# Optimization experiments

Hardware: AMD Instinct MI355X
Metric: run time of the kernel (lower is better)

## Reference

```python
import jax, jax.numpy as jnp
import numpy as np

N = 50000        # nodes
E = 800000       # edges (before self-loops)
IN = 128         # in_dim
H = 2            # heads
C1 = 64          # hidden_dim (per head)
D1 = H * C1      # conv1 concat output = 128
OUT = 64         # out_dim
C2 = 2 * OUT     # conv2 per-head channels = 128 (concat=False -> mean over heads)
NEG = 0.2        # GATv2 leaky_relu negative slope
EPS = 1e-5       # BatchNorm eps


def setup_inputs() -> dict:
    key = jax.random.key(0)
    ks = jax.random.split(key, 14)
    s = 0.05
    inp = {
        "x": jax.random.normal(ks[0], (N, IN), jnp.float32),
        "edge_index": jax.random.randint(ks[1], (2, E), 0, N, dtype=jnp.int32),
        # conv1 (GATv2: lin_l for source, lin_r for target, att vector per head)
        "W_l1": jax.random.normal(ks[2], (IN, D1), jnp.float32) * s,
        "b_l1": jnp.zeros((D1,), jnp.float32),
        "W_r1": jax.random.normal(ks[3], (IN, D1), jnp.float32) * s,
        "b_r1": jnp.zeros((D1,), jnp.float32),
        "att1": jax.random.normal(ks[4], (H, C1), jnp.float32) * s,
        "bias1": jnp.zeros((D1,), jnp.float32),
        # batch_norm1 (affine)
        "gamma1": jnp.ones((D1,), jnp.float32),
        "beta1": jnp.zeros((D1,), jnp.float32),
        # conv2
        "W_l2": jax.random.normal(ks[5], (D1, H * C2), jnp.float32) * s,
        "b_l2": jnp.zeros((H * C2,), jnp.float32),
        "W_r2": jax.random.normal(ks[6], (D1, H * C2), jnp.float32) * s,
        "b_r2": jnp.zeros((H * C2,), jnp.float32),
        "att2": jax.random.normal(ks[7], (H, C2), jnp.float32) * s,
        "bias2": jnp.zeros((C2,), jnp.float32),
    }
    return inp


def gatv2_layer(x, src, dst, W_l, b_l, W_r, b_r, att, bias, concat):
    Hh, Cc = att.shape
    x_l = (x @ W_l + b_l).reshape(N, Hh, Cc)   # source transform
    x_r = (x @ W_r + b_r).reshape(N, Hh, Cc)   # target transform
    # per-edge GATv2 score: att . leaky_relu(x_l[j] + x_r[i])
    e = jax.nn.leaky_relu(x_l[src] + x_r[dst], NEG)      # [E', H, C]
    logit = jnp.einsum("ehc,hc->eh", e, att)              # [E', H]
    # segment softmax over incoming edges of each target node
    m = jax.ops.segment_max(logit, dst, num_segments=N)   # [N, H]
    ex = jnp.exp(logit - m[dst])
    den = jax.ops.segment_sum(ex, dst, num_segments=N)    # [N, H]
    alpha = ex / den[dst]                                  # [E', H]
    out = jax.ops.segment_sum(x_l[src] * alpha[:, :, None], dst, num_segments=N)
    out = out.reshape(N, Hh * Cc) if concat else out.mean(axis=1)
    return out + bias


def batchnorm(x, gamma=None, beta=None):
    mu = x.mean(axis=0)
    var = x.var(axis=0)  # biased variance, as used by BN for normalization
    xn = (x - mu) * jax.lax.rsqrt(var + EPS)
    if gamma is not None:
        xn = xn * gamma + beta
    return xn


def reference(x, edge_index, W_l1, b_l1, W_r1, b_r1, att1, bias1, gamma1, beta1,
              W_l2, b_l2, W_r2, b_r2, att2, bias2):
    loops = jnp.arange(N, dtype=edge_index.dtype)
    src = jnp.concatenate([edge_index[0], loops])  # add self-loops (PyG default)
    dst = jnp.concatenate([edge_index[1], loops])
    h = gatv2_layer(x, src, dst, W_l1, b_l1, W_r1, b_r1, att1, bias1, True)
    h = jax.nn.relu(batchnorm(h, gamma1, beta1))
    o = gatv2_layer(h, src, dst, W_l2, b_l2, W_r2, b_r2, att2, bias2, False)
    mu_part = batchnorm(o[:, :OUT])                      # affine=False
    return jnp.concatenate([mu_part, jax.nn.softplus(o[:, OUT:])], axis=1)
```

## Files before the change

kernel.cpp:

```cpp
#include <hip/hip_runtime.h>
#include <hip/hip_bf16.h>
#include <math.h>

#define NNODES 50000
#define NEDGES 800000
#define EPTOT  (NEDGES + NNODES)
#define NEG_SLOPE 0.2f
#define BN_EPS 1e-5f
#define LOG2E 1.44269504088896f
#define ESLOT 64

#define PB_SC  3321
#define PB_W1  (PB_SC + 128)
#define PB_W2  (PB_W1 + 256)

typedef __hip_bfloat16 bf16;
typedef __attribute__((ext_vector_type(8))) short short8;
typedef __attribute__((ext_vector_type(4))) float f32x4;
typedef __attribute__((ext_vector_type(2))) float f32x2;

__device__ __forceinline__ unsigned short f2us(float f){
    return (unsigned short)(__bfloat16_as_ushort(__float2bfloat16(f)));
}
__device__ __forceinline__ f32x2 unpk(unsigned int w){
    union { unsigned int u; float f; } lo, hi;
    lo.u = w << 16; hi.u = w & 0xffff0000u;
    f32x2 r; r.x = lo.f; r.y = hi.f; return r;
}
__device__ __forceinline__ f32x2 pkmax(f32x2 a, f32x2 b){
#if __has_builtin(__builtin_elementwise_max)
    return __builtin_elementwise_max(a, b);
#else
    f32x2 r; r.x = fmaxf(a.x, b.x); r.y = fmaxf(a.y, b.y); return r;
#endif
}
__device__ __forceinline__ unsigned int pack2(float a, float b){
    return (unsigned int)f2us(a) | ((unsigned int)f2us(b) << 16);
}


__global__ __launch_bounds__(256) void misc_prep(
    const int* __restrict__ ei, int* __restrict__ cnt, int* __restrict__ esrc,
    const float* __restrict__ Wl1, const float* __restrict__ Wr1,
    const float* __restrict__ bl1, const float* __restrict__ br1,
    bf16* __restrict__ WT1, float* __restrict__ bc1,
    const float* __restrict__ Wl2, const float* __restrict__ Wr2,
    const float* __restrict__ bl2, const float* __restrict__ br2,
    bf16* __restrict__ WT2, float* __restrict__ bc2)
{
    int b = blockIdx.x;
    if (b < PB_SC){
        int e = b * 256 + threadIdx.x;
        if (e < EPTOT){
            int s, d;
            if (e < NEDGES){ s = ei[e]; d = ei[NEDGES + e]; } else { s = d = e - NEDGES; }
            int pos = atomicAdd(&cnt[d], 1);
            if (pos < ESLOT) esrc[(d << 6) + pos] = s;
        }
    } else if (b < PB_W1){
        int i = (b - PB_SC) * 256 + threadIdx.x;
        int r = i >> 7, k = i & 127;
        const float* W = (r < 128) ? Wl1 : Wr1;
        int c = (r < 128) ? r : r - 128;
        WT1[i] = __float2bfloat16(W[k * 128 + c]);
        if (k == 0) bc1[r] = (r < 128) ? bl1[c] : br1[c];
    } else {
        int i = (b - PB_W1) * 256 + threadIdx.x;
        int r = i >> 7, k = i & 127;
        const float* W = (r < 256) ? Wl2 : Wr2;
        int c = (r < 256) ? r : r - 256;
        WT2[i] = __float2bfloat16(W[k * 256 + c]);
        if (k == 0) bc2[r] = (r < 256) ? bl2[c] : br2[c];
    }
}


template<int DTOT, bool F32A, int NT>
__global__ __launch_bounds__(128) void mfma_gemm(
    const void* __restrict__ A, const bf16* __restrict__ WT,
    const float* __restrict__ biascat,
    bf16* __restrict__ xl, bf16* __restrict__ xr)
{
    int wave = threadIdx.x >> 6;
    int lane = threadIdx.x & 63;
    int quad = lane >> 4;
    int l16  = lane & 15;
    int m0 = blockIdx.x * 128 + wave * 64;
    const short* Ap = (const short*)A;
    const float* Af = (const float*)A;
    const short* Bp = (const short*)WT;

    short8 af[4][4];
    #pragma unroll
    for (int k = 0; k < 4; ++k)
        #pragma unroll
        for (int mt = 0; mt < 4; ++mt){
            int m = m0 + mt * 16 + l16;
            m = (m < NNODES) ? m : (NNODES - 1);
            if (F32A){
                float4 v0 = *(const float4*)(Af + (size_t)m * 128 + k * 32 + quad * 8);
                float4 v1 = *(const float4*)(Af + (size_t)m * 128 + k * 32 + quad * 8 + 4);
                unsigned int* u = (unsigned int*)&af[k][mt];
                u[0] = pack2(v0.x, v0.y); u[1] = pack2(v0.z, v0.w);
                u[2] = pack2(v1.x, v1.y); u[3] = pack2(v1.z, v1.w);
            } else {
                af[k][mt] = *(const short8*)(Ap + (size_t)m * 128 + k * 32 + quad * 8);
            }
        }

    for (int t = 0; t < NT; ++t){
        int n0 = (blockIdx.y * NT + t) * 64;
        f32x4 acc[4][4] = {};
        #pragma unroll
        for (int k = 0; k < 4; ++k){
            short8 bfr[4];
            #pragma unroll
            for (int nt = 0; nt < 4; ++nt){
                int n = n0 + nt * 16 + l16;
                bfr[nt] = *(const short8*)(Bp + (size_t)n * 128 + k * 32 + quad * 8);
            }
            #pragma unroll
            for (int mt = 0; mt < 4; ++mt)
                #pragma unroll
                for (int nt = 0; nt < 4; ++nt)
                    acc[mt][nt] = __builtin_amdgcn_mfma_f32_16x16x32_bf16(af[k][mt], bfr[nt], acc[mt][nt], 0, 0, 0);
        }
        #pragma unroll
        for (int nt = 0; nt < 4; ++nt){
            int n = n0 + nt * 16 + l16;
            float bi = biascat[n];
            bf16* outp = (n < DTOT) ? xl : xr;
            int c = (n < DTOT) ? n : n - DTOT;
            #pragma unroll
            for (int mt = 0; mt < 4; ++mt)
                #pragma unroll
                for (int r = 0; r < 4; ++r){
                    int m = m0 + mt * 16 + quad * 4 + r;
                    if (m < NNODES)
                        outp[(size_t)m * DTOT + c] = __float2bfloat16(acc[mt][nt][r] + bi);
                }
        }
    }
}


template<int C, bool MEAN>
__global__ __launch_bounds__(128) void gat_aggregate(
    const bf16* __restrict__ xl, const bf16* __restrict__ xr,
    const float* __restrict__ att, const int* __restrict__ cnt,
    const int* __restrict__ esrc, void* __restrict__ outv,
    const float* __restrict__ bias2)
{
    constexpr int G  = C / 8;
    constexpr int E  = 64 / G;
    constexpr int HC = 2 * C;
    __shared__ float tmp[HC];
    int n    = blockIdx.x;
    int lane = threadIdx.x & 63;
    int head = threadIdx.x >> 6;
    int g    = lane / G;
    int cl   = lane % G;
    int rowoff = head * (C * 2) + cl * 16;
    const char* xlp = (const char*)xl;

    int srcAll = esrc[(n << 6) + lane];
    int cc = cnt[n];
    int c = (cc < ESLOT) ? cc : ESLOT;
    uint4 xw = *(const uint4*)((const char*)xr + (unsigned)(n * (HC * 2) + rowoff));
    f32x2 xr0 = unpk(xw.x), xr1 = unpk(xw.y), xr2v = unpk(xw.z), xr3 = unpk(xw.w);
    const float* ap = att + head * C + cl * 8;
    f32x2 av0 = {ap[0] * LOG2E, ap[1] * LOG2E};
    f32x2 av1 = {ap[2] * LOG2E, ap[3] * LOG2E};
    f32x2 av2 = {ap[4] * LOG2E, ap[5] * LOG2E};
    f32x2 av3 = {ap[6] * LOG2E, ap[7] * LOG2E};

    float den = 0.f;
    f32x2 a0 = {0.f,0.f}, a1 = {0.f,0.f}, a2 = {0.f,0.f}, a3 = {0.f,0.f};

    int p = 0;
    for (; p + E < c; p += 2 * E){
        int ib = p + E + g;
        int sa = __shfl(srcAll, p + g, 64);
        int sb = __shfl(srcAll, (ib < c) ? ib : (c - 1), 64);
        float mkb = (ib < c) ? 0.f : -1e30f;
        uint4 wa = *(const uint4*)(xlp + ((unsigned)sa * (unsigned)(HC * 2) + rowoff));
        uint4 wb = *(const uint4*)(xlp + ((unsigned)sb * (unsigned)(HC * 2) + rowoff));

        f32x2 xa0 = unpk(wa.x), xa1 = unpk(wa.y), xa2 = unpk(wa.z), xa3 = unpk(wa.w);
        f32x2 xb0 = unpk(wb.x), xb1 = unpk(wb.y), xb2 = unpk(wb.z), xb3 = unpk(wb.w);

        f32x2 ua0 = xa0 + xr0, ua1 = xa1 + xr1, ua2 = xa2 + xr2v, ua3 = xa3 + xr3;
        f32x2 ub0 = xb0 + xr0, ub1 = xb1 + xr1, ub2 = xb2 + xr2v, ub3 = xb3 + xr3;

        f32x2 ppa = pkmax(ua0, ua0 * NEG_SLOPE) * av0;
        ppa += pkmax(ua1, ua1 * NEG_SLOPE) * av1;
        ppa += pkmax(ua2, ua2 * NEG_SLOPE) * av2;
        ppa += pkmax(ua3, ua3 * NEG_SLOPE) * av3;
        f32x2 ppb = pkmax(ub0, ub0 * NEG_SLOPE) * av0;
        ppb += pkmax(ub1, ub1 * NEG_SLOPE) * av1;
        ppb += pkmax(ub2, ub2 * NEG_SLOPE) * av2;
        ppb += pkmax(ub3, ub3 * NEG_SLOPE) * av3;
        float parta = ppa.x + ppa.y;
        float partb = ppb.x + ppb.y;
        #pragma unroll
        for (int mask = G / 2; mask >= 1; mask >>= 1){
            parta += __shfl_xor(parta, mask, 64);
            partb += __shfl_xor(partb, mask, 64);
        }
        float exa = exp2f(parta);
        float exb = exp2f(partb + mkb);
        den += exa + exb;
        f32x2 ea = {exa, exa}, eb = {exb, exb};
        a0 += ea * xa0; a1 += ea * xa1; a2 += ea * xa2; a3 += ea * xa3;
        a0 += eb * xb0; a1 += eb * xb1; a2 += eb * xb2; a3 += eb * xb3;
    }
    if (p < c){
        int ia = p + g;
        int sa = __shfl(srcAll, (ia < c) ? ia : (c - 1), 64);
        float mka = (ia < c) ? 0.f : -1e30f;
        uint4 wa = *(const uint4*)(xlp + ((unsigned)sa * (unsigned)(HC * 2) + rowoff));

        f32x2 xa0 = unpk(wa.x), xa1 = unpk(wa.y), xa2 = unpk(wa.z), xa3 = unpk(wa.w);
        f32x2 ua0 = xa0 + xr0, ua1 = xa1 + xr1, ua2 = xa2 + xr2v, ua3 = xa3 + xr3;

        f32x2 ppa = pkmax(ua0, ua0 * NEG_SLOPE) * av0;
        ppa += pkmax(ua1, ua1 * NEG_SLOPE) * av1;
        ppa += pkmax(ua2, ua2 * NEG_SLOPE) * av2;
        ppa += pkmax(ua3, ua3 * NEG_SLOPE) * av3;
        float parta = ppa.x + ppa.y;
        #pragma unroll
        for (int mask = G / 2; mask >= 1; mask >>= 1)
            parta += __shfl_xor(parta, mask, 64);
        float exa = exp2f(parta + mka);
        den += exa;
        f32x2 ea = {exa, exa};
        a0 += ea * xa0; a1 += ea * xa1; a2 += ea * xa2; a3 += ea * xa3;
    }

    #pragma unroll
    for (int mask = G; mask < 64; mask <<= 1){
        den  += __shfl_xor(den, mask, 64);
        a0.x += __shfl_xor(a0.x, mask, 64); a0.y += __shfl_xor(a0.y, mask, 64);
        a1.x += __shfl_xor(a1.x, mask, 64); a1.y += __shfl_xor(a1.y, mask, 64);
        a2.x += __shfl_xor(a2.x, mask, 64); a2.y += __shfl_xor(a2.y, mask, 64);
        a3.x += __shfl_xor(a3.x, mask, 64); a3.y += __shfl_xor(a3.y, mask, 64);
    }
    float inv = 1.f / den;

    if (!MEAN){
        if (g == 0){
            uint4 o;
            o.x = pack2(a0.x * inv, a0.y * inv);
            o.y = pack2(a1.x * inv, a1.y * inv);
            o.z = pack2(a2.x * inv, a2.y * inv);
            o.w = pack2(a3.x * inv, a3.y * inv);
            *(uint4*)((char*)outv + (size_t)n * (HC * 2) + rowoff) = o;
        }
    } else {
        if (g == 0){
            float* tp = tmp + head * C + cl * 8;
            tp[0] = a0.x * inv; tp[1] = a0.y * inv;
            tp[2] = a1.x * inv; tp[3] = a1.y * inv;
            tp[4] = a2.x * inv; tp[5] = a2.y * inv;
            tp[6] = a3.x * inv; tp[7] = a3.y * inv;
        }
        __syncthreads();
        if (head == 0 && g == 0){
            float* outp = (float*)outv + (size_t)n * C;
            #pragma unroll
            for (int v = 0; v < 8; ++v){
                int c2 = cl * 8 + v;
                outp[c2] = 0.5f * (tmp[c2] + tmp[C + c2]) + bias2[c2];
            }
        }
    }
}


__global__ void bn_stats_bf16(const unsigned int* __restrict__ x, float* __restrict__ sums){
    __shared__ float ls[1024];
    int t = threadIdx.x;
    int c2 = t & 63;
    int rg = t >> 6;
    float s0 = 0.f, q0 = 0.f, s1 = 0.f, q1 = 0.f;
    for (int r = blockIdx.x * 4 + rg; r < NNODES; r += gridDim.x * 4){
        f32x2 v = unpk(x[(size_t)r * 64 + c2]);
        s0 += v.x; q0 += v.x * v.x;
        s1 += v.y; q1 += v.y * v.y;
    }
    ls[t] = s0; ls[256 + t] = q0; ls[512 + t] = s1; ls[768 + t] = q1;
    __syncthreads();
    if (rg == 0){
        for (int g = 1; g < 4; ++g){
            s0 += ls[g * 64 + c2];       q0 += ls[256 + g * 64 + c2];
            s1 += ls[512 + g * 64 + c2]; q1 += ls[768 + g * 64 + c2];
        }
        atomicAdd(&sums[2 * c2], s0);
        atomicAdd(&sums[128 + 2 * c2], q0);
        atomicAdd(&sums[2 * c2 + 1], s1);
        atomicAdd(&sums[128 + 2 * c2 + 1], q1);
    }
}

__global__ void bn_stats_o2(const float* __restrict__ x, float* __restrict__ sums){
    __shared__ float ls[512];
    int t = threadIdx.x;
    int col = t & 63;
    int rg  = t >> 6;
    float s = 0.f, q = 0.f;
    for (int r = blockIdx.x * 4 + rg; r < NNODES; r += gridDim.x * 4){
        float v = x[(size_t)r * 128 + col];
        s += v; q += v * v;
    }
    ls[t] = s; ls[256 + t] = q;
    __syncthreads();
    if (rg == 0){
        for (int g = 1; g < 4; ++g){ s += ls[g * 64 + col]; q += ls[256 + g * 64 + col]; }
        atomicAdd(&sums[col], s);
        atomicAdd(&sums[64 + col], q);
    }
}

__global__ void bn_apply_relu(const unsigned int* __restrict__ o1, const float* __restrict__ sums,
                              const float* __restrict__ gamma, const float* __restrict__ beta,
                              unsigned int* __restrict__ h){
    int i = blockIdx.x * blockDim.x + threadIdx.x;
    if (i >= NNODES * 64) return;
    int c2 = i & 63;
    int c0 = 2 * c2, c1 = c0 + 1;
    const float inv_n = 1.f / (float)NNODES;
    float mu0 = sums[c0] * inv_n;
    float sc0 = gamma[c0] * rsqrtf(sums[128 + c0] * inv_n - mu0 * mu0 + BN_EPS);
    float sh0 = beta[c0] - mu0 * sc0;
    float mu1 = sums[c1] * inv_n;
    float sc1 = gamma[c1] * rsqrtf(sums[128 + c1] * inv_n - mu1 * mu1 + BN_EPS);
    float sh1 = beta[c1] - mu1 * sc1;
    f32x2 v = unpk(o1[i]);
    float v0 = v.x * sc0 + sh0;
    float v1 = v.y * sc1 + sh1;
    h[i] = pack2(v0 > 0.f ? v0 : 0.f, v1 > 0.f ? v1 : 0.f);
}

__global__ void final_out(const float* __restrict__ o2, const float* __restrict__ sums,
                          float* __restrict__ out){
    int i = blockIdx.x * blockDim.x + threadIdx.x;
    if (i >= NNODES * 32) return;
    float4 v = *(const float4*)(o2 + (size_t)i * 4);
    int c = (i * 4) & 127;
    const float* vp = (const float*)&v;
    float4 r;
    float* rp = (float*)&r;
    if (c < 64){
        const float inv_n = 1.f / (float)NNODES;
        #pragma unroll
        for (int k = 0; k < 4; ++k){
            float mu = sums[c + k] * inv_n;
            float rsig = rsqrtf(sums[64 + c + k] * inv_n - mu * mu + BN_EPS);
            rp[k] = (vp[k] - mu) * rsig;
        }
    } else {
        #pragma unroll
        for (int k = 0; k < 4; ++k){
            float x = vp[k];
            rp[k] = (x > 20.f) ? x : log1pf(__expf(x));
        }
    }
    *(float4*)(out + (size_t)i * 4) = r;
}


extern "C" void kernel_launch(void* const* d_in, const int* in_sizes, int n_in,
                              void* d_out, int out_size, void* d_ws, size_t ws_size,
                              hipStream_t stream) {
    const float* x     = (const float*)d_in[0];
    const int*   ei    = (const int*)d_in[1];
    const float* W_l1  = (const float*)d_in[2];
    const float* b_l1  = (const float*)d_in[3];
    const float* W_r1  = (const float*)d_in[4];
    const float* b_r1  = (const float*)d_in[5];
    const float* att1  = (const float*)d_in[6];
    const float* gamma1 = (const float*)d_in[8];
    const float* beta1  = (const float*)d_in[9];
    const float* W_l2  = (const float*)d_in[10];
    const float* b_l2  = (const float*)d_in[11];
    const float* W_r2  = (const float*)d_in[12];
    const float* b_r2  = (const float*)d_in[13];
    const float* att2  = (const float*)d_in[14];
    const float* bias2 = (const float*)d_in[15];
    float* out = (float*)d_out;

    char* w = (char*)d_ws;
    size_t off = 0;
    auto alloc = [&](size_t bytes) -> void* {
        void* p = w + off;
        off += (bytes + 255) & ~(size_t)255;
        return p;
    };
    const size_t NF  = (size_t)NNODES * 128 * 4;
    bf16*  xl1   = (bf16*) alloc(NF / 2);
    bf16*  xr1   = (bf16*) alloc(NF / 2);
    bf16*  xl2   = (bf16*) alloc(NF);
    bf16*  xr2   = (bf16*) alloc(NF);
    bf16*  hbuf  = (bf16*) alloc(NF / 2);
    unsigned int* o1 = (unsigned int*)alloc(NF / 2);
    float* o2    = (float*)alloc(NF);
    bf16*  WT1   = (bf16*) alloc(256 * 128 * 2);
    bf16*  WT2   = (bf16*) alloc(512 * 128 * 2);
    float* bc1   = (float*)alloc(256 * 4);
    float* bc2   = (float*)alloc(512 * 4);
    int*   cnt    = (int*)  alloc((size_t)NNODES * 4);
    int*   esrc   = (int*)  alloc((size_t)NNODES * ESLOT * 4);
    float* bnsums = (float*)alloc(384 * 4);
    float* bn1s = bnsums;
    float* bn2s = bnsums + 256;

    hipMemsetAsync(cnt, 0, (size_t)NNODES * 4, stream);
    hipMemsetAsync(bnsums, 0, 384 * 4, stream);

    misc_prep<<<PB_W2, 256, 0, stream>>>(ei, cnt, esrc,
                                         W_l1, W_r1, b_l1, b_r1, WT1, bc1,
                                         W_l2, W_r2, b_l2, b_r2, WT2, bc2);

    mfma_gemm<128, true, 2><<<dim3(392, 2), 128, 0, stream>>>(x, WT1, bc1, xl1, xr1);
    gat_aggregate<64, false><<<NNODES, 128, 0, stream>>>(xl1, xr1, att1, cnt, esrc, o1, bias2);

    bn_stats_bf16<<<512, 256, 0, stream>>>(o1, bn1s);
    bn_apply_relu<<<(NNODES * 64 + 255) / 256, 256, 0, stream>>>(o1, bn1s, gamma1, beta1, (unsigned int*)hbuf);

    mfma_gemm<256, false, 2><<<dim3(392, 4), 128, 0, stream>>>(hbuf, WT2, bc2, xl2, xr2);
    gat_aggregate<128, true><<<NNODES, 128, 0, stream>>>(xl2, xr2, att2, cnt, esrc, o2, bias2);

    bn_stats_o2<<<512, 256, 0, stream>>>(o2, bn2s);
    final_out<<<(NNODES * 32 + 255) / 256, 256, 0, stream>>>(o2, bn2s, out);
}
```

Baseline: 425.3 us.

## Make GAT aggregate persistent grid-stride with next-node metadata prefetch

The aggregation kernels change from one block per node to a fixed grid of 4096 blocks that stride over the nodes. Each iteration prefetches the next node's edge list, degree and target row while the current node is processed. Attention and bias constants are loaded once per block, and shared memory is double-buffered so the mean path needs only one barrier per node. The aim is to cut block launch overhead and hide metadata load latency, at the cost of possible load imbalance and less latency hiding from a smaller number of resident blocks.

```diff
diff --git a/kernel.cpp b/kernel.cpp
--- a/kernel.cpp
+++ b/kernel.cpp
@@ -9,6 +9,7 @@
 #define BN_EPS 1e-5f
 #define LOG2E 1.44269504088896f
 #define ESLOT 64
+#define AGG_GRID 4096
 
 #define PB_SC  3321
 #define PB_W1  (PB_SC + 128)
@@ -154,125 +155,146 @@
     constexpr int G  = C / 8;
     constexpr int E  = 64 / G;
     constexpr int HC = 2 * C;
-    __shared__ float tmp[HC];
-    int n    = blockIdx.x;
+    __shared__ float tmp[2][HC];
     int lane = threadIdx.x & 63;
     int head = threadIdx.x >> 6;
     int g    = lane / G;
     int cl   = lane % G;
     int rowoff = head * (C * 2) + cl * 16;
     const char* xlp = (const char*)xl;
-
-    int srcAll = esrc[(n << 6) + lane];
-    int cc = cnt[n];
-    int c = (cc < ESLOT) ? cc : ESLOT;
-    uint4 xw = *(const uint4*)((const char*)xr + (unsigned)(n * (HC * 2) + rowoff));
-    f32x2 xr0 = unpk(xw.x), xr1 = unpk(xw.y), xr2v = unpk(xw.z), xr3 = unpk(xw.w);
+    const char* xrp = (const char*)xr;
+
     const float* ap = att + head * C + cl * 8;
     f32x2 av0 = {ap[0] * LOG2E, ap[1] * LOG2E};
     f32x2 av1 = {ap[2] * LOG2E, ap[3] * LOG2E};
     f32x2 av2 = {ap[4] * LOG2E, ap[5] * LOG2E};
     f32x2 av3 = {ap[6] * LOG2E, ap[7] * LOG2E};
-
-    float den = 0.f;
-    f32x2 a0 = {0.f,0.f}, a1 = {0.f,0.f}, a2 = {0.f,0.f}, a3 = {0.f,0.f};
-
-    int p = 0;
-    for (; p + E < c; p += 2 * E){
-        int ib = p + E + g;
-        int sa = __shfl(srcAll, p + g, 64);
-        int sb = __shfl(srcAll, (ib < c) ? ib : (c - 1), 64);
-        float mkb = (ib < c) ? 0.f : -1e30f;
-        uint4 wa = *(const uint4*)(xlp + ((unsigned)sa * (unsigned)(HC * 2) + rowoff));
-        uint4 wb = *(const uint4*)(xlp + ((unsigned)sb * (unsigned)(HC * 2) + rowoff));
-
-        f32x2 xa0 = unpk(wa.x), xa1 = unpk(wa.y), xa2 = unpk(wa.z), xa3 = unpk(wa.w);
-        f32x2 xb0 = unpk(wb.x), xb1 = unpk(wb.y), xb2 = unpk(wb.z), xb3 = unpk(wb.w);
-
-        f32x2 ua0 = xa0 + xr0, ua1 = xa1 + xr1, ua2 = xa2 + xr2v, ua3 = xa3 + xr3;
-        f32x2 ub0 = xb0 + xr0, ub1 = xb1 + xr1, ub2 = xb2 + xr2v, ub3 = xb3 + xr3;
-
-        f32x2 ppa = pkmax(ua0, ua0 * NEG_SLOPE) * av0;
-        ppa += pkmax(ua1, ua1 * NEG_SLOPE) * av1;
-        ppa += pkmax(ua2, ua2 * NEG_SLOPE) * av2;
-        ppa += pkmax(ua3, ua3 * NEG_SLOPE) * av3;
-        f32x2 ppb = pkmax(ub0, ub0 * NEG_SLOPE) * av0;
-        ppb += pkmax(ub1, ub1 * NEG_SLOPE) * av1;
-        ppb += pkmax(ub2, ub2 * NEG_SLOPE) * av2;
-        ppb += pkmax(ub3, ub3 * NEG_SLOPE) * av3;
-        float parta = ppa.x + ppa.y;
-        float partb = ppb.x + ppb.y;
-        #pragma unroll
-        for (int mask = G / 2; mask >= 1; mask >>= 1){
-            parta += __shfl_xor(parta, mask, 64);
-            partb += __shfl_xor(partb, mask, 64);
-        }
-        float exa = exp2f(parta);
-        float exb = exp2f(partb + mkb);
-        den += exa + exb;
-        f32x2 ea = {exa, exa}, eb = {exb, exb};
-        a0 += ea * xa0; a1 += ea * xa1; a2 += ea * xa2; a3 += ea * xa3;
-        a0 += eb * xb0; a1 += eb * xb1; a2 += eb * xb2; a3 += eb * xb3;
-    }
-    if (p < c){
-        int ia = p + g;
-        int sa = __shfl(srcAll, (ia < c) ? ia : (c - 1), 64);
-        float mka = (ia < c) ? 0.f : -1e30f;
-        uint4 wa = *(const uint4*)(xlp + ((unsigned)sa * (unsigned)(HC * 2) + rowoff));
-
-        f32x2 xa0 = unpk(wa.x), xa1 = unpk(wa.y), xa2 = unpk(wa.z), xa3 = unpk(wa.w);
-        f32x2 ua0 = xa0 + xr0, ua1 = xa1 + xr1, ua2 = xa2 + xr2v, ua3 = xa3 + xr3;
-
-        f32x2 ppa = pkmax(ua0, ua0 * NEG_SLOPE) * av0;
-        ppa += pkmax(ua1, ua1 * NEG_SLOPE) * av1;
-        ppa += pkmax(ua2, ua2 * NEG_SLOPE) * av2;
-        ppa += pkmax(ua3, ua3 * NEG_SLOPE) * av3;
-        float parta = ppa.x + ppa.y;
-        #pragma unroll
-        for (int mask = G / 2; mask >= 1; mask >>= 1)
-            parta += __shfl_xor(parta, mask, 64);
-        float exa = exp2f(parta + mka);
-        den += exa;
-        f32x2 ea = {exa, exa};
-        a0 += ea * xa0; a1 += ea * xa1; a2 += ea * xa2; a3 += ea * xa3;
-    }
-
-    #pragma unroll
-    for (int mask = G; mask < 64; mask <<= 1){
-        den  += __shfl_xor(den, mask, 64);
-        a0.x += __shfl_xor(a0.x, mask, 64); a0.y += __shfl_xor(a0.y, mask, 64);
-        a1.x += __shfl_xor(a1.x, mask, 64); a1.y += __shfl_xor(a1.y, mask, 64);
-        a2.x += __shfl_xor(a2.x, mask, 64); a2.y += __shfl_xor(a2.y, mask, 64);
-        a3.x += __shfl_xor(a3.x, mask, 64); a3.y += __shfl_xor(a3.y, mask, 64);
-    }
-    float inv = 1.f / den;
-
-    if (!MEAN){
-        if (g == 0){
-            uint4 o;
-            o.x = pack2(a0.x * inv, a0.y * inv);
-            o.y = pack2(a1.x * inv, a1.y * inv);
-            o.z = pack2(a2.x * inv, a2.y * inv);
-            o.w = pack2(a3.x * inv, a3.y * inv);
-            *(uint4*)((char*)outv + (size_t)n * (HC * 2) + rowoff) = o;
-        }
-    } else {
-        if (g == 0){
-            float* tp = tmp + head * C + cl * 8;
-            tp[0] = a0.x * inv; tp[1] = a0.y * inv;
-            tp[2] = a1.x * inv; tp[3] = a1.y * inv;
-            tp[4] = a2.x * inv; tp[5] = a2.y * inv;
-            tp[6] = a3.x * inv; tp[7] = a3.y * inv;
-        }
-        __syncthreads();
-        if (head == 0 && g == 0){
-            float* outp = (float*)outv + (size_t)n * C;
+    float b2r[8];
+    if (MEAN){
+        #pragma unroll
+        for (int v = 0; v < 8; ++v) b2r[v] = bias2[cl * 8 + v];
+    }
+
+    int n = blockIdx.x;
+    if (n >= NNODES) return;
+    int  srcAll = esrc[(n << 6) + lane];
+    int  cc     = cnt[n];
+    uint4 xw    = *(const uint4*)(xrp + (unsigned)n * (HC * 2) + rowoff);
+    int par = 0;
+
+    while (n < NNODES){
+        int n2  = n + AGG_GRID;
+        int npf = (n2 < NNODES) ? n2 : n;
+        int  srcAll2 = esrc[(npf << 6) + lane];
+        int  cc2     = cnt[npf];
+        uint4 xw2    = *(const uint4*)(xrp + (unsigned)npf * (HC * 2) + rowoff);
+
+        int c = (cc < ESLOT) ? cc : ESLOT;
+        f32x2 xr0 = unpk(xw.x), xr1 = unpk(xw.y), xr2v = unpk(xw.z), xr3 = unpk(xw.w);
+
+        float den = 0.f;
+        f32x2 a0 = {0.f,0.f}, a1 = {0.f,0.f}, a2 = {0.f,0.f}, a3 = {0.f,0.f};
+
+        int p = 0;
+        for (; p + E < c; p += 2 * E){
+            int ib = p + E + g;
+            int sa = __shfl(srcAll, p + g, 64);
+            int sb = __shfl(srcAll, (ib < c) ? ib : (c - 1), 64);
+            float mkb = (ib < c) ? 0.f : -1e30f;
+            uint4 wa = *(const uint4*)(xlp + ((unsigned)sa * (unsigned)(HC * 2) + rowoff));
+            uint4 wb = *(const uint4*)(xlp + ((unsigned)sb * (unsigned)(HC * 2) + rowoff));
+
+            f32x2 xa0 = unpk(wa.x), xa1 = unpk(wa.y), xa2 = unpk(wa.z), xa3 = unpk(wa.w);
+            f32x2 xb0 = unpk(wb.x), xb1 = unpk(wb.y), xb2 = unpk(wb.z), xb3 = unpk(wb.w);
+
+            f32x2 ua0 = xa0 + xr0, ua1 = xa1 + xr1, ua2 = xa2 + xr2v, ua3 = xa3 + xr3;
+            f32x2 ub0 = xb0 + xr0, ub1 = xb1 + xr1, ub2 = xb2 + xr2v, ub3 = xb3 + xr3;
+
+            f32x2 ppa = pkmax(ua0, ua0 * NEG_SLOPE) * av0;
+            ppa += pkmax(ua1, ua1 * NEG_SLOPE) * av1;
+            ppa += pkmax(ua2, ua2 * NEG_SLOPE) * av2;
+            ppa += pkmax(ua3, ua3 * NEG_SLOPE) * av3;
+            f32x2 ppb = pkmax(ub0, ub0 * NEG_SLOPE) * av0;
+            ppb += pkmax(ub1, ub1 * NEG_SLOPE) * av1;
+            ppb += pkmax(ub2, ub2 * NEG_SLOPE) * av2;
+            ppb += pkmax(ub3, ub3 * NEG_SLOPE) * av3;
+            float parta = ppa.x + ppa.y;
+            float partb = ppb.x + ppb.y;
             #pragma unroll
-            for (int v = 0; v < 8; ++v){
-                int c2 = cl * 8 + v;
-                outp[c2] = 0.5f * (tmp[c2] + tmp[C + c2]) + bias2[c2];
-            }
-        }
+            for (int mask = G / 2; mask >= 1; mask >>= 1){
+                parta += __shfl_xor(parta, mask, 64);
+                partb += __shfl_xor(partb, mask, 64);
+            }
+            float exa = exp2f(parta);
+            float exb = exp2f(partb + mkb);
+            den += exa + exb;
+            f32x2 ea = {exa, exa}, eb = {exb, exb};
+            a0 += ea * xa0; a1 += ea * xa1; a2 += ea * xa2; a3 += ea * xa3;
+            a0 += eb * xb0; a1 += eb * xb1; a2 += eb * xb2; a3 += eb * xb3;
+        }
+        if (p < c){
+            int ia = p + g;
+            int sa = __shfl(srcAll, (ia < c) ? ia : (c - 1), 64);
+            float mka = (ia < c) ? 0.f : -1e30f;
+            uint4 wa = *(const uint4*)(xlp + ((unsigned)sa * (unsigned)(HC * 2) + rowoff));
+
+            f32x2 xa0 = unpk(wa.x), xa1 = unpk(wa.y), xa2 = unpk(wa.z), xa3 = unpk(wa.w);
+            f32x2 ua0 = xa0 + xr0, ua1 = xa1 + xr1, ua2 = xa2 + xr2v, ua3 = xa3 + xr3;
+
+            f32x2 ppa = pkmax(ua0, ua0 * NEG_SLOPE) * av0;
+            ppa += pkmax(ua1, ua1 * NEG_SLOPE) * av1;
+            ppa += pkmax(ua2, ua2 * NEG_SLOPE) * av2;
+            ppa += pkmax(ua3, ua3 * NEG_SLOPE) * av3;
+            float parta = ppa.x + ppa.y;
+            #pragma unroll
+            for (int mask = G / 2; mask >= 1; mask >>= 1)
+                parta += __shfl_xor(parta, mask, 64);
+            float exa = exp2f(parta + mka);
+            den += exa;
+            f32x2 ea = {exa, exa};
+            a0 += ea * xa0; a1 += ea * xa1; a2 += ea * xa2; a3 += ea * xa3;
+        }
+
+        #pragma unroll
+        for (int mask = G; mask < 64; mask <<= 1){
+            den  += __shfl_xor(den, mask, 64);
+            a0.x += __shfl_xor(a0.x, mask, 64); a0.y += __shfl_xor(a0.y, mask, 64);
+            a1.x += __shfl_xor(a1.x, mask, 64); a1.y += __shfl_xor(a1.y, mask, 64);
+            a2.x += __shfl_xor(a2.x, mask, 64); a2.y += __shfl_xor(a2.y, mask, 64);
+            a3.x += __shfl_xor(a3.x, mask, 64); a3.y += __shfl_xor(a3.y, mask, 64);
+        }
+        float inv = 1.f / den;
+
+        if (!MEAN){
+            if (g == 0){
+                uint4 o;
+                o.x = pack2(a0.x * inv, a0.y * inv);
+                o.y = pack2(a1.x * inv, a1.y * inv);
+                o.z = pack2(a2.x * inv, a2.y * inv);
+                o.w = pack2(a3.x * inv, a3.y * inv);
+                *(uint4*)((char*)outv + (size_t)n * (HC * 2) + rowoff) = o;
+            }
+        } else {
+            if (g == 0){
+                float* tp = &tmp[par][head * C + cl * 8];
+                tp[0] = a0.x * inv; tp[1] = a0.y * inv;
+                tp[2] = a1.x * inv; tp[3] = a1.y * inv;
+                tp[4] = a2.x * inv; tp[5] = a2.y * inv;
+                tp[6] = a3.x * inv; tp[7] = a3.y * inv;
+            }
+            __syncthreads();
+            if (head == 0 && g == 0){
+                float* outp = (float*)outv + (size_t)n * C;
+                #pragma unroll
+                for (int v = 0; v < 8; ++v){
+                    int c2 = cl * 8 + v;
+                    outp[c2] = 0.5f * (tmp[par][c2] + tmp[par][C + c2]) + b2r[v];
+                }
+            }
+            par ^= 1;
+        }
+
+        n = n2; srcAll = srcAll2; cc = cc2; xw = xw2;
     }
 }
 
@@ -422,13 +444,13 @@
                                          W_l2, W_r2, b_l2, b_r2, WT2, bc2);
 
     mfma_gemm<128, true, 2><<<dim3(392, 2), 128, 0, stream>>>(x, WT1, bc1, xl1, xr1);
-    gat_aggregate<64, false><<<NNODES, 128, 0, stream>>>(xl1, xr1, att1, cnt, esrc, o1, bias2);
+    gat_aggregate<64, false><<<AGG_GRID, 128, 0, stream>>>(xl1, xr1, att1, cnt, esrc, o1, bias2);
 
     bn_stats_bf16<<<512, 256, 0, stream>>>(o1, bn1s);
     bn_apply_relu<<<(NNODES * 64 + 255) / 256, 256, 0, stream>>>(o1, bn1s, gamma1, beta1, (unsigned int*)hbuf);
 
     mfma_gemm<256, false, 2><<<dim3(392, 4), 128, 0, stream>>>(hbuf, WT2, bc2, xl2, xr2);
-    gat_aggregate<128, true><<<NNODES, 128, 0, stream>>>(xl2, xr2, att2, cnt, esrc, o2, bias2);
+    gat_aggregate<128, true><<<AGG_GRID, 128, 0, stream>>>(xl2, xr2, att2, cnt, esrc, o2, bias2);
 
     bn_stats_o2<<<512, 256, 0, stream>>>(o2, bn2s);
     final_out<<<(NNODES * 32 + 255) / 256, 256, 0, stream>>>(o2, bn2s, out);
```

Measured after the change: 459.6 us. +8.1%, slower.
